# Kernel tuning notes

Hardware: AMD Instinct MI355X
Metric: run time of the kernel (lower is better)

## Reference

```python
import jax, jax.numpy as jnp
import numpy as np

LAMBDA_COORD = 5.0
LAMBDA_NOOBJ = 0.5
EPS = 1e-9


def _bbox_iou(px, py, pr, gx, gy, gr):
    """IoU of the axis-aligned bounding squares of two circles (x, y, r)."""
    l1, r1, t1, b1 = px - pr, px + pr, py - pr, py + pr
    l2, r2, t2, b2 = gx - gr, gx + gr, gy - gr, gy + gr
    iw = jnp.maximum(jnp.minimum(r1, r2) - jnp.maximum(l1, l2), 0.0)
    ih = jnp.maximum(jnp.minimum(b1, b2) - jnp.maximum(t1, t2), 0.0)
    inter = iw * ih
    a1 = (r1 - l1) * (b1 - t1)
    a2 = (r2 - l2) * (b2 - t2)
    return inter / (a1 + a2 - inter + EPS)


def setup_inputs() -> dict:
    key = jax.random.key(0)
    k1, k2, k3, k4 = jax.random.split(key, 4)
    B, L, G, C = 65536, 16, 8, 8
    pred = jax.random.uniform(k1, (B, G, G, C), dtype=jnp.float32)
    label_rc = jax.random.randint(k2, (B, L, 2), 0, G, dtype=jnp.int32)
    xy = jax.random.uniform(k3, (B, L, 2), dtype=jnp.float32)
    r = jax.random.uniform(k4, (B, L, 1), dtype=jnp.float32) * 0.2 + 0.01
    label_box = jnp.concatenate([xy, r], axis=-1)
    return {"pred": pred, "label_rc": label_rc, "label_box": label_box}


def reference(pred, label_rc, label_box):
    B = pred.shape[0]
    rows = label_rc[..., 0]  # [B, L]
    cols = label_rc[..., 1]
    bidx = jnp.arange(B)[:, None]
    pb = pred[bidx, rows, cols]  # [B, L, 8] responsible cell per label

    gx, gy, gr = label_box[..., 0], label_box[..., 1], label_box[..., 2]
    iou1 = _bbox_iou(pb[..., 0], pb[..., 1], pb[..., 2], gx, gy, gr)
    iou2 = _bbox_iou(pb[..., 4], pb[..., 5], pb[..., 6], gx, gy, gr)

    swap = iou2 > iou1
    cx = jnp.where(swap, pb[..., 4], pb[..., 0])
    cy = jnp.where(swap, pb[..., 5], pb[..., 1])
    cr = jnp.where(swap, pb[..., 6], pb[..., 2])
    conf = jnp.where(swap, pb[..., 7], pb[..., 3])
    un_conf = jnp.where(swap, pb[..., 3], pb[..., 7])
    bigger = jnp.where(swap, iou2, iou1)
    smaller = jnp.where(swap, iou1, iou2)

    coord_loss = LAMBDA_COORD * jnp.sum(
        (cx - gx) ** 2 + (cy - gy) ** 2 + (cr - gr) ** 2)
    cond_loss = jnp.sum((bigger - conf) ** 2)
    cond_loss = cond_loss + LAMBDA_NOOBJ * jnp.sum((smaller - un_conf) ** 2)

    # object mask over the 8x8 grid (duplicates collapse to 1, as in original)
    obj_mask = jnp.zeros(pred.shape[:3], dtype=pred.dtype).at[bidx, rows, cols].set(1.0)
    noobj = (pred[..., 3] ** 2 + pred[..., 7] ** 2) * (1.0 - obj_mask)
    cond_loss = cond_loss + LAMBDA_NOOBJ * jnp.sum(noobj)

    return (coord_loss + cond_loss) / B
```

## Files before the change

### kernel.cpp

```cpp
#include <hip/hip_runtime.h>


static constexpr float LAMBDA_COORD = 5.0f;
static constexpr float LAMBDA_NOOBJ = 0.5f;
static constexpr float EPS_F = 1e-9f;

__device__ __forceinline__ float bbox_iou(float px, float py, float pr,
                                          float gx, float gy, float gr) {
    float l1 = px - pr, r1 = px + pr, t1 = py - pr, b1 = py + pr;
    float l2 = gx - gr, r2 = gx + gr, t2 = gy - gr, b2 = gy + gr;
    float iw = fmaxf(fminf(r1, r2) - fmaxf(l1, l2), 0.0f);
    float ih = fmaxf(fminf(b1, b2) - fmaxf(t1, t2), 0.0f);
    float inter = iw * ih;
    float a1 = (r1 - l1) * (b1 - t1);
    float a2 = (r2 - l2) * (b2 - t2);
    return inter / (a1 + a2 - inter + EPS_F);
}

__global__ __launch_bounds__(256) void yolo_loss_kernel(
    const float* __restrict__ pred,
    const int*   __restrict__ label_rc,
    const float* __restrict__ label_box,
    float* __restrict__ partials,
    int B, int L)
{
    const int lane    = threadIdx.x & 63;
    const int wave_ib = threadIdx.x >> 6;
    const int b       = blockIdx.x * 4 + wave_ib;

    float contrib = 0.0f;

    if (b < B) {
        const float* cell_ptr = pred + ((size_t)b << 9) + ((size_t)lane << 3);
        float4 q0 = *(const float4*)(cell_ptr);
        float4 q1 = *(const float4*)(cell_ptr + 4);

        int   cell = -1;
        float gx = 0.f, gy = 0.f, gr = 0.f;
        if (lane < L) {
            const int2 rc = *(const int2*)(label_rc + ((size_t)b * L + lane) * 2);
            cell = rc.x * 8 + rc.y;
            const float* lb = label_box + ((size_t)b * L + lane) * 3;
            gx = lb[0]; gy = lb[1]; gr = lb[2];
        }

        bool labeled = false;
        #pragma unroll
        for (int l = 0; l < 16; ++l) {
            if (l < L) labeled |= (__shfl(cell, l) == lane);
        }

        int src = (cell < 0) ? 0 : cell;
        float p0 = __shfl(q0.x, src);
        float p1 = __shfl(q0.y, src);
        float p2 = __shfl(q0.z, src);
        float p3 = __shfl(q0.w, src);
        float p4 = __shfl(q1.x, src);
        float p5 = __shfl(q1.y, src);
        float p6 = __shfl(q1.z, src);
        float p7 = __shfl(q1.w, src);

        contrib = labeled ? 0.0f
                : LAMBDA_NOOBJ * (q0.w * q0.w + q1.w * q1.w);

        if (lane < L) {
            float iou1 = bbox_iou(p0, p1, p2, gx, gy, gr);
            float iou2 = bbox_iou(p4, p5, p6, gx, gy, gr);
            bool  sw   = iou2 > iou1;
            float cx      = sw ? p4 : p0;
            float cy      = sw ? p5 : p1;
            float cr      = sw ? p6 : p2;
            float conf    = sw ? p7 : p3;
            float un_conf = sw ? p3 : p7;
            float bigger  = sw ? iou2 : iou1;
            float smaller = sw ? iou1 : iou2;
            float dx = cx - gx, dy = cy - gy, dr = cr - gr;
            contrib += LAMBDA_COORD * (dx * dx + dy * dy + dr * dr);
            float d1 = bigger - conf;
            float d2 = smaller - un_conf;
            contrib += d1 * d1 + LAMBDA_NOOBJ * (d2 * d2);
        }
    }

    #pragma unroll
    for (int off = 32; off > 0; off >>= 1)
        contrib += __shfl_xor(contrib, off);

    __shared__ float wsum[4];
    if (lane == 0) wsum[wave_ib] = contrib;
    __syncthreads();
    if (threadIdx.x == 0)
        partials[blockIdx.x] = wsum[0] + wsum[1] + wsum[2] + wsum[3];
}

__global__ __launch_bounds__(256) void reduce_kernel(
    const float* __restrict__ partials, float* __restrict__ out,
    int n4, float invB)
{
    const float4* p4 = (const float4*)partials;
    float4 s4 = make_float4(0.f, 0.f, 0.f, 0.f);
    for (int i = threadIdx.x; i < n4; i += 256) {
        float4 v = p4[i];
        s4.x += v.x; s4.y += v.y; s4.z += v.z; s4.w += v.w;
    }
    float s = (s4.x + s4.y) + (s4.z + s4.w);
    #pragma unroll
    for (int off = 32; off > 0; off >>= 1)
        s += __shfl_xor(s, off);

    __shared__ float wsum[4];
    const int lane = threadIdx.x & 63, w = threadIdx.x >> 6;
    if (lane == 0) wsum[w] = s;
    __syncthreads();
    if (threadIdx.x == 0)
        out[0] = (wsum[0] + wsum[1] + wsum[2] + wsum[3]) * invB;
}

extern "C" void kernel_launch(void* const* d_in, const int* in_sizes, int n_in,
                              void* d_out, int out_size, void* d_ws, size_t ws_size,
                              hipStream_t stream) {
    const float* pred      = (const float*)d_in[0];
    const int*   label_rc  = (const int*)d_in[1];
    const float* label_box = (const float*)d_in[2];
    float*       out       = (float*)d_out;
    float*       partials  = (float*)d_ws;

    const int B = in_sizes[0] / 512;
    const int L = in_sizes[1] / (B * 2);
    const float invB = 1.0f / (float)B;

    const int blocks = (B + 3) / 4;
    yolo_loss_kernel<<<blocks, 256, 0, stream>>>(
        pred, label_rc, label_box, partials, B, L);

    reduce_kernel<<<1, 256, 0, stream>>>(partials, out, blocks / 4, invB);
}
```

Before: 207.8 us.

## Split YOLO loss into label-gather blocks and a streaming no-object reduction

The single kernel is split into two kinds of blocks in one launch. Label blocks handle four batch items per wave, 16 lanes each, and gather each responsible cell directly from global memory. A shared-memory atomicMin marks which label owns each cell so its no-object term is subtracted only once. The remaining blocks stream over all cells with a grid-stride loop, four loads in flight, and accumulate the squared confidence values. This removes the per-wave full-row load, the shuffle-based label matching and the lanes left idle when L is 16, at the cost of re-reading the gathered cells and issuing strided single-dword loads.

```diff
diff --git a/kernel.cpp b/kernel.cpp
--- a/kernel.cpp
+++ b/kernel.cpp
@@ -17,53 +17,53 @@
     return inter / (a1 + a2 - inter + EPS_F);
 }
 
-__global__ __launch_bounds__(256) void yolo_loss_kernel(
+__global__ __launch_bounds__(256) void yolo_loss_fused(
     const float* __restrict__ pred,
     const int*   __restrict__ label_rc,
     const float* __restrict__ label_box,
     float* __restrict__ partials,
-    int B, int L)
+    int B, int L, int nbB, int nbA)
 {
     const int lane    = threadIdx.x & 63;
     const int wave_ib = threadIdx.x >> 6;
-    const int b       = blockIdx.x * 4 + wave_ib;
 
-    float contrib = 0.0f;
+    __shared__ unsigned int owner[4][256];
+    __shared__ float wsum[4];
 
-    if (b < B) {
-        const float* cell_ptr = pred + ((size_t)b << 9) + ((size_t)lane << 3);
-        float4 q0 = *(const float4*)(cell_ptr);
-        float4 q1 = *(const float4*)(cell_ptr + 4);
+    float acc = 0.0f;
 
-        int   cell = -1;
+    if ((int)blockIdx.x < nbB) {
+        const int sub = lane >> 4;
+        const int ll  = lane & 15;
+        const int wave_id = blockIdx.x * 4 + wave_ib;
+        const int b = wave_id * 4 + sub;
+
+        #pragma unroll
+        for (int k = 0; k < 4; ++k)
+            owner[wave_ib][k * 64 + lane] = 0xFFFFFFFFu;
+
+        const bool active = (b < B) && (ll < L);
+        int   cell = 0;
         float gx = 0.f, gy = 0.f, gr = 0.f;
-        if (lane < L) {
-            const int2 rc = *(const int2*)(label_rc + ((size_t)b * L + lane) * 2);
+        float4 g0 = make_float4(0.f, 0.f, 0.f, 0.f);
+        float4 g1 = g0;
+
+        if (active) {
+            const int2 rc = *(const int2*)(label_rc + ((size_t)b * L + ll) * 2);
             cell = rc.x * 8 + rc.y;
-            const float* lb = label_box + ((size_t)b * L + lane) * 3;
+            const float* lb = label_box + ((size_t)b * L + ll) * 3;
             gx = lb[0]; gy = lb[1]; gr = lb[2];
+            const float4* gp =
+                (const float4*)(pred + ((size_t)b << 9) + ((size_t)cell << 3));
+            g0 = gp[0];
+            g1 = gp[1];
+            atomicMin(&owner[wave_ib][sub * 64 + cell], (unsigned)ll);
         }
 
-        bool labeled = false;
-        #pragma unroll
-        for (int l = 0; l < 16; ++l) {
-            if (l < L) labeled |= (__shfl(cell, l) == lane);
-        }
+        if (active) {
+            const float p0 = g0.x, p1 = g0.y, p2 = g0.z, p3 = g0.w;
+            const float p4 = g1.x, p5 = g1.y, p6 = g1.z, p7 = g1.w;
 
-        int src = (cell < 0) ? 0 : cell;
-        float p0 = __shfl(q0.x, src);
-        float p1 = __shfl(q0.y, src);
-        float p2 = __shfl(q0.z, src);
-        float p3 = __shfl(q0.w, src);
-        float p4 = __shfl(q1.x, src);
-        float p5 = __shfl(q1.y, src);
-        float p6 = __shfl(q1.z, src);
-        float p7 = __shfl(q1.w, src);
-
-        contrib = labeled ? 0.0f
-                : LAMBDA_NOOBJ * (q0.w * q0.w + q1.w * q1.w);
-
-        if (lane < L) {
             float iou1 = bbox_iou(p0, p1, p2, gx, gy, gr);
             float iou2 = bbox_iou(p4, p5, p6, gx, gy, gr);
             bool  sw   = iou2 > iou1;
@@ -75,19 +75,40 @@
             float bigger  = sw ? iou2 : iou1;
             float smaller = sw ? iou1 : iou2;
             float dx = cx - gx, dy = cy - gy, dr = cr - gr;
-            contrib += LAMBDA_COORD * (dx * dx + dy * dy + dr * dr);
+            acc += LAMBDA_COORD * (dx * dx + dy * dy + dr * dr);
             float d1 = bigger - conf;
             float d2 = smaller - un_conf;
-            contrib += d1 * d1 + LAMBDA_NOOBJ * (d2 * d2);
+            acc += d1 * d1 + LAMBDA_NOOBJ * (d2 * d2);
+
+            if (owner[wave_ib][sub * 64 + cell] == (unsigned)ll)
+                acc -= LAMBDA_NOOBJ * (p3 * p3 + p7 * p7);
         }
+    } else {
+        const int aBlock = (int)blockIdx.x - nbB;
+        const float4* pv = (const float4*)pred;
+        const size_t N4 = (size_t)B * 128;
+        const size_t stride = (size_t)nbA * 256;
+        size_t i = (size_t)aBlock * 256 + threadIdx.x;
+
+        float a0 = 0.f, a1 = 0.f, a2 = 0.f, a3 = 0.f;
+        for (; i + 3 * stride < N4; i += 4 * stride) {
+            float w0 = pv[i].w;
+            float w1 = pv[i + stride].w;
+            float w2 = pv[i + 2 * stride].w;
+            float w3 = pv[i + 3 * stride].w;
+            a0 += w0 * w0; a1 += w1 * w1; a2 += w2 * w2; a3 += w3 * w3;
+        }
+        for (; i < N4; i += stride) {
+            float w = pv[i].w; a0 += w * w;
+        }
+        acc = LAMBDA_NOOBJ * ((a0 + a1) + (a2 + a3));
     }
 
     #pragma unroll
     for (int off = 32; off > 0; off >>= 1)
-        contrib += __shfl_xor(contrib, off);
+        acc += __shfl_xor(acc, off);
 
-    __shared__ float wsum[4];
-    if (lane == 0) wsum[wave_ib] = contrib;
+    if (lane == 0) wsum[wave_ib] = acc;
     __syncthreads();
     if (threadIdx.x == 0)
         partials[blockIdx.x] = wsum[0] + wsum[1] + wsum[2] + wsum[3];
@@ -129,9 +150,12 @@
     const int L = in_sizes[1] / (B * 2);
     const float invB = 1.0f / (float)B;
 
-    const int blocks = (B + 3) / 4;
-    yolo_loss_kernel<<<blocks, 256, 0, stream>>>(
-        pred, label_rc, label_box, partials, B, L);
+    const int nbB = (B + 15) / 16;
+    const int nbA = 8192;
+    const int total = nbB + nbA;
 
-    reduce_kernel<<<1, 256, 0, stream>>>(partials, out, blocks / 4, invB);
+    yolo_loss_fused<<<total, 256, 0, stream>>>(
+        pred, label_rc, label_box, partials, B, L, nbB, nbA);
+
+    reduce_kernel<<<1, 256, 0, stream>>>(partials, out, total / 4, invB);
 }
```

Result: no change. 211.5 us (+1.8%).

## Stage 16 batches per block in LDS and dedupe labeled cells via atomicMin

Applied to the files above, without the earlier changes.

Each block now handles 16 batch items instead of 4. It loads all of their predictions into shared memory with fully coalesced float4 loads and adds the no-object term for every cell unconditionally. It then maps one thread per label so all 256 threads do useful label work, rather than only 16 of 64 lanes per wave. Labeled cells are deduplicated with an LDS atomicMin owner table, and the owner subtracts the no-object term back out. This costs 32KB+4KB of LDS per block, which limits occupancy, and adds extra barriers; the reduce kernel now reads four times fewer partials.

```diff
diff --git a/kernel.cpp b/kernel.cpp
--- a/kernel.cpp
+++ b/kernel.cpp
@@ -17,6 +17,8 @@
     return inter / (a1 + a2 - inter + EPS_F);
 }
 
+#define W_BATCH 16
+
 __global__ __launch_bounds__(256) void yolo_loss_kernel(
     const float* __restrict__ pred,
     const int*   __restrict__ label_rc,
@@ -24,86 +26,101 @@
     float* __restrict__ partials,
     int B, int L)
 {
-    const int lane    = threadIdx.x & 63;
-    const int wave_ib = threadIdx.x >> 6;
-    const int b       = blockIdx.x * 4 + wave_ib;
+    __shared__ float        sp[W_BATCH * 512];
+    __shared__ unsigned int owner[W_BATCH * 64];
+    __shared__ float        wsum[4];
 
-    float contrib = 0.0f;
+    const int tid = threadIdx.x;
+    const int b0  = blockIdx.x * W_BATCH;
+    const int nb  = min(W_BATCH, B - b0);
 
-    if (b < B) {
-        const float* cell_ptr = pred + ((size_t)b << 9) + ((size_t)lane << 3);
-        float4 q0 = *(const float4*)(cell_ptr);
-        float4 q1 = *(const float4*)(cell_ptr + 4);
+    #pragma unroll
+    for (int k = 0; k < 4; ++k)
+        owner[k * 256 + tid] = 0xFFFFFFFFu;
 
-        int   cell = -1;
-        float gx = 0.f, gy = 0.f, gr = 0.f;
-        if (lane < L) {
-            const int2 rc = *(const int2*)(label_rc + ((size_t)b * L + lane) * 2);
-            cell = rc.x * 8 + rc.y;
-            const float* lb = label_box + ((size_t)b * L + lane) * 3;
-            gx = lb[0]; gy = lb[1]; gr = lb[2];
+    const float4* gp = (const float4*)(pred + (size_t)b0 * 512);
+    float4*       sv = (float4*)sp;
+    const int     n4 = nb * 128;
+
+    float acc = 0.0f;
+    if (nb == W_BATCH) {
+        float4 v[8];
+        #pragma unroll
+        for (int k = 0; k < 8; ++k) v[k] = gp[k * 256 + tid];
+        #pragma unroll
+        for (int k = 0; k < 8; ++k) {
+            acc += v[k].w * v[k].w;
+            sv[k * 256 + tid] = v[k];
         }
-
-        bool labeled = false;
-        #pragma unroll
-        for (int l = 0; l < 16; ++l) {
-            if (l < L) labeled |= (__shfl(cell, l) == lane);
-        }
-
-        int src = (cell < 0) ? 0 : cell;
-        float p0 = __shfl(q0.x, src);
-        float p1 = __shfl(q0.y, src);
-        float p2 = __shfl(q0.z, src);
-        float p3 = __shfl(q0.w, src);
-        float p4 = __shfl(q1.x, src);
-        float p5 = __shfl(q1.y, src);
-        float p6 = __shfl(q1.z, src);
-        float p7 = __shfl(q1.w, src);
-
-        contrib = labeled ? 0.0f
-                : LAMBDA_NOOBJ * (q0.w * q0.w + q1.w * q1.w);
-
-        if (lane < L) {
-            float iou1 = bbox_iou(p0, p1, p2, gx, gy, gr);
-            float iou2 = bbox_iou(p4, p5, p6, gx, gy, gr);
-            bool  sw   = iou2 > iou1;
-            float cx      = sw ? p4 : p0;
-            float cy      = sw ? p5 : p1;
-            float cr      = sw ? p6 : p2;
-            float conf    = sw ? p7 : p3;
-            float un_conf = sw ? p3 : p7;
-            float bigger  = sw ? iou2 : iou1;
-            float smaller = sw ? iou1 : iou2;
-            float dx = cx - gx, dy = cy - gy, dr = cr - gr;
-            contrib += LAMBDA_COORD * (dx * dx + dy * dy + dr * dr);
-            float d1 = bigger - conf;
-            float d2 = smaller - un_conf;
-            contrib += d1 * d1 + LAMBDA_NOOBJ * (d2 * d2);
+    } else {
+        for (int i = tid; i < n4; i += 256) {
+            float4 v = gp[i];
+            acc += v.w * v.w;
+            sv[i] = v;
         }
     }
+    acc *= LAMBDA_NOOBJ;
+    __syncthreads();
+
+    int   cell = -1, w = 0;
+    float p3 = 0.f, p7 = 0.f;
+    if (tid < nb * L) {
+        w = tid / L;
+        const int l = tid - w * L;
+        const int b = b0 + w;
+
+        const int2 rc = *(const int2*)(label_rc + ((size_t)b * L + l) * 2);
+        cell = rc.x * 8 + rc.y;
+        atomicMin(&owner[w * 64 + cell], (unsigned)tid);
+
+        const float* lb = label_box + ((size_t)b * L + l) * 3;
+        const float gx = lb[0], gy = lb[1], gr = lb[2];
+
+        const float4* cp = (const float4*)(sp + w * 512 + cell * 8);
+        const float4 c0 = cp[0];
+        const float4 c1 = cp[1];
+        const float p0 = c0.x, p1 = c0.y, p2 = c0.z;
+        const float p4 = c1.x, p5 = c1.y, p6 = c1.z;
+        p3 = c0.w; p7 = c1.w;
+
+        float iou1 = bbox_iou(p0, p1, p2, gx, gy, gr);
+        float iou2 = bbox_iou(p4, p5, p6, gx, gy, gr);
+        bool  sw   = iou2 > iou1;
+        float cx      = sw ? p4 : p0;
+        float cy      = sw ? p5 : p1;
+        float cr      = sw ? p6 : p2;
+        float conf    = sw ? p7 : p3;
+        float un_conf = sw ? p3 : p7;
+        float bigger  = sw ? iou2 : iou1;
+        float smaller = sw ? iou1 : iou2;
+        float dx = cx - gx, dy = cy - gy, dr = cr - gr;
+        acc += LAMBDA_COORD * (dx * dx + dy * dy + dr * dr);
+        float d1 = bigger - conf;
+        float d2 = smaller - un_conf;
+        acc += d1 * d1 + LAMBDA_NOOBJ * (d2 * d2);
+    }
+    __syncthreads();
+
+    if (cell >= 0 && owner[w * 64 + cell] == (unsigned)tid)
+        acc -= LAMBDA_NOOBJ * (p3 * p3 + p7 * p7);
 
     #pragma unroll
     for (int off = 32; off > 0; off >>= 1)
-        contrib += __shfl_xor(contrib, off);
-
-    __shared__ float wsum[4];
-    if (lane == 0) wsum[wave_ib] = contrib;
+        acc += __shfl_xor(acc, off);
+    const int lane = tid & 63, wv = tid >> 6;
+    if (lane == 0) wsum[wv] = acc;
     __syncthreads();
-    if (threadIdx.x == 0)
+    if (tid == 0)
         partials[blockIdx.x] = wsum[0] + wsum[1] + wsum[2] + wsum[3];
 }
 
 __global__ __launch_bounds__(256) void reduce_kernel(
     const float* __restrict__ partials, float* __restrict__ out,
-    int n4, float invB)
+    int n, float invB)
 {
-    const float4* p4 = (const float4*)partials;
-    float4 s4 = make_float4(0.f, 0.f, 0.f, 0.f);
-    for (int i = threadIdx.x; i < n4; i += 256) {
-        float4 v = p4[i];
-        s4.x += v.x; s4.y += v.y; s4.z += v.z; s4.w += v.w;
-    }
-    float s = (s4.x + s4.y) + (s4.z + s4.w);
+    float s = 0.0f;
+    for (int i = threadIdx.x; i < n; i += 256)
+        s += partials[i];
     #pragma unroll
     for (int off = 32; off > 0; off >>= 1)
         s += __shfl_xor(s, off);
@@ -129,9 +146,9 @@
     const int L = in_sizes[1] / (B * 2);
     const float invB = 1.0f / (float)B;
 
-    const int blocks = (B + 3) / 4;
+    const int blocks = (B + W_BATCH - 1) / W_BATCH;
     yolo_loss_kernel<<<blocks, 256, 0, stream>>>(
         pred, label_rc, label_box, partials, B, L);
 
-    reduce_kernel<<<1, 256, 0, stream>>>(partials, out, blocks / 4, invB);
+    reduce_kernel<<<1, 256, 0, stream>>>(partials, out, blocks, invB);
 }
```

Result: no change. 205.4 us (-1.1%).
